# Kernel tuning notes

Measured on AMD Instinct MI355X. Metric: run time of the kernel, lower is better.

## Reference

```python
import jax, jax.numpy as jnp
from jax import lax
import numpy as np

VOCAB, HIDDEN, NUM_TAGS = 8000, 256, 4
B, T = 128, 512


def setup_inputs() -> dict:
    key = jax.random.key(0)
    ks = jax.random.split(key, 12)
    s_emb = 1.0
    s_conv = 1.0 / np.sqrt(HIDDEN * 3)
    s_dense = 1.0 / np.sqrt(HIDDEN)
    emb = jax.random.normal(ks[0], (VOCAB, HIDDEN), jnp.float32) * s_emb
    emb = emb.at[0].set(0.0)  # padding_idx=0
    inp = {
        'x': jax.random.randint(ks[1], (B, T), 0, VOCAB, jnp.int32),
        'y': jax.random.randint(ks[2], (B, T), 0, NUM_TAGS, jnp.int32),
        'mask': jnp.ones((B, T), jnp.bool_),
        'emb': emb,
        'w1': jax.random.normal(ks[3], (HIDDEN, HIDDEN, 3), jnp.float32) * s_conv,
        'b1': jnp.zeros((HIDDEN,), jnp.float32),
        'w2': jax.random.normal(ks[4], (HIDDEN, HIDDEN, 3), jnp.float32) * s_conv,
        'b2': jnp.zeros((HIDDEN,), jnp.float32),
        'w3': jax.random.normal(ks[5], (HIDDEN, HIDDEN, 3), jnp.float32) * s_conv,
        'b3': jnp.zeros((HIDDEN,), jnp.float32),
        'dense_w': jax.random.normal(ks[6], (NUM_TAGS, HIDDEN), jnp.float32) * s_dense,
        'dense_b': jnp.zeros((NUM_TAGS,), jnp.float32),
        'start_trans': jax.random.uniform(ks[7], (NUM_TAGS,), jnp.float32, -0.1, 0.1),
        'end_trans': jax.random.uniform(ks[8], (NUM_TAGS,), jnp.float32, -0.1, 0.1),
        'trans': jax.random.uniform(ks[9], (NUM_TAGS, NUM_TAGS), jnp.float32, -0.1, 0.1),
    }
    return inp


def _conv_relu(h, w, b):
    # h: [B, C, T]; replicate-pad 1 each side on time, kernel 3, stride 1
    hp = jnp.pad(h, ((0, 0), (0, 0), (1, 1)), mode='edge')
    out = lax.conv_general_dilated(hp, w, (1,), 'VALID',
                                   dimension_numbers=('NCH', 'OIH', 'NCH'))
    return jax.nn.relu(out + b[None, :, None])


def _crf_llh(em, tags, mask, start_trans, end_trans, trans):
    # em [B,T,L], tags [B,T], mask [B,T] float -> summed log-likelihood (torchcrf reduction='sum')
    bsz = em.shape[0]
    em_t = jnp.swapaxes(em, 0, 1)      # [T,B,L]
    tags_t = tags.T                    # [T,B]
    mask_t = mask.T                    # [T,B]
    bidx = jnp.arange(bsz)

    # numerator: score of the given tag sequence
    first = start_trans[tags_t[0]] + em_t[0, bidx, tags_t[0]]

    def num_step(carry, inp):
        score, prev = carry
        e, tg, m = inp
        s = trans[prev, tg] + e[bidx, tg]
        score = score + s * m
        prev = jnp.where(m > 0, tg, prev)
        return (score, prev), None

    (num, last_tag), _ = lax.scan(num_step, (first, tags_t[0]),
                                  (em_t[1:], tags_t[1:], mask_t[1:]))
    num = num + end_trans[last_tag]

    # denominator: forward algorithm (log partition)
    alpha0 = start_trans[None, :] + em_t[0]  # [B,L]

    def part_step(alpha, inp):
        e, m = inp
        nxt = jax.nn.logsumexp(alpha[:, :, None] + trans[None, :, :] + e[:, None, :], axis=1)
        return jnp.where(m[:, None] > 0, nxt, alpha), None

    alpha, _ = lax.scan(part_step, alpha0, (em_t[1:], mask_t[1:]))
    logz = jax.nn.logsumexp(alpha + end_trans[None, :], axis=1)
    return jnp.sum(num - logz)


def reference(x, y, mask, emb, w1, b1, w2, b2, w3, b3, dense_w, dense_b,
              start_trans, end_trans, trans):
    h = emb[x]                         # [B,T,H]
    h = jnp.swapaxes(h, 1, 2)          # [B,H,T]
    h = _conv_relu(h, w1, b1)
    h = _conv_relu(h, w2, b2)
    h = _conv_relu(h, w3, b3)
    h = jnp.swapaxes(h, 1, 2)          # [B,T,H]
    em = jnp.einsum('bth,lh->btl', h, dense_w) + dense_b
    m = mask.astype(em.dtype)
    return _crf_llh(em, y, m, start_trans, end_trans, trans)
```

## Files before the change

kernel.cpp:

```cpp
#include <hip/hip_runtime.h>
#include <hip/hip_bf16.h>
#include <hip/hip_fp8.h>

#define Bc 128
#define Tt 512
#define Hc 256
#define Lc 4
#define BM 128
#define APB 272
#define HR 134

typedef __attribute__((ext_vector_type(8))) short short8;
typedef __attribute__((ext_vector_type(4))) float f32x4;
typedef unsigned char uchar;
typedef unsigned long long u64;

__device__ __forceinline__ uchar f2f8(float f) {
    __hip_fp8_e4m3 q(f);
    return (uchar)q.__x;
}
__device__ __forceinline__ float f82f(uchar b) {
    __hip_fp8_e4m3 q; q.__x = (__hip_fp8_storage_t)b;
    return (float)q;
}

__global__ __launch_bounds__(256) void prep_emb(const float* __restrict__ e,
                                                uchar* __restrict__ eb)
{
    int i = blockIdx.x * 256 + threadIdx.x;
    const float4* s = (const float4*)(e + (size_t)i * 8);
    float4 a = s[0], b = s[1];
    u64 r = (u64)f2f8(a.x)
          | ((u64)f2f8(a.y) << 8)
          | ((u64)f2f8(a.z) << 16)
          | ((u64)f2f8(a.w) << 24)
          | ((u64)f2f8(b.x) << 32)
          | ((u64)f2f8(b.y) << 40)
          | ((u64)f2f8(b.z) << 48)
          | ((u64)f2f8(b.w) << 56);
    *(u64*)(eb + (size_t)i * 8) = r;
}

__global__ __launch_bounds__(256) void prep_w(const float* __restrict__ w,
                                              uchar* __restrict__ wbF)
{
    int i = blockIdx.x * 256 + threadIdx.x;
    int co = i / 768;
    int r  = i - co * 768;
    int ci = r / 3;
    int k  = r - ci * 3;
    int cib = ci >> 5, lk = (ci >> 3) & 3, e = ci & 7;
    wbF[(size_t)(k * 8 + cib) * 8192 + co * 32 + lk * 8 + e] = f2f8(w[i]);
}

__global__ __launch_bounds__(512) void fused_net(
    const uchar* __restrict__ embF, const int* __restrict__ x,
    const uchar* __restrict__ wbF,
    const float* __restrict__ b1, const float* __restrict__ b2,
    const float* __restrict__ b3,
    const float* __restrict__ dw, const float* __restrict__ db,
    float* __restrict__ em)
{
    __shared__ __align__(16) uchar Hb[HR * APB];

    const int b    = blockIdx.y;
    const int t0   = blockIdx.x * BM;
    const int tid  = threadIdx.x;
    const int lane = tid & 63, wid = tid >> 6;
    const int wm = wid >> 2, wn = wid & 3;
    const int lr = lane & 15, lk = lane >> 4;
    const bool first = (blockIdx.x == 0), last = (blockIdx.x == gridDim.x - 1);

    for (int ch = tid; ch < HR * 16; ch += 512) {
        int r = ch >> 4, c = ch & 15;
        int t = t0 - 3 + r;
        t = t < 0 ? 0 : (t > Tt - 1 ? Tt - 1 : t);
        int row = x[b * Tt + t];
        *(short8*)&Hb[r * APB + c * 16] =
            *(const short8*)&embF[(size_t)row * Hc + c * 16];
    }
    __syncthreads();

    const int blo = wn * 2048 + lr * 32 + lk * 8;
    const f32x4 fzero = {0.f, 0.f, 0.f, 0.f};

    for (int layer = 0; layer < 3; ++layer) {
        const uchar* wL = wbF + (size_t)layer * 24 * 8192;
        const float* bz = layer == 0 ? b1 : (layer == 1 ? b2 : b3);

        int ob[5];
        #pragma unroll
        for (int f = 0; f < 4; ++f) ob[f] = (1 + layer) + (wm * 4 + f) * 16;
        ob[4] = 117 - layer;

        f32x4 acc[5][4];
        #pragma unroll
        for (int f = 0; f < 5; ++f)
            #pragma unroll
            for (int ni = 0; ni < 4; ++ni) acc[f][ni] = fzero;

        long bp[3][4];
        #pragma unroll
        for (int ni = 0; ni < 4; ++ni)
            bp[0][ni] = *(const long*)&wL[blo + ni * 512];
        #pragma unroll
        for (int ni = 0; ni < 4; ++ni)
            bp[1][ni] = *(const long*)&wL[8192 + blo + ni * 512];

        long af[2][5];
        #pragma unroll
        for (int f = 0; f < 5; ++f)
            af[0][f] = *(const long*)&Hb[(ob[f] + lr - 1) * APB + lk * 8];

        #pragma unroll
        for (int s = 0; s < 24; ++s) {
            const int cur = s & 1;
            if (s + 2 < 24) {
                const uchar* nb = wL + (size_t)(s + 2) * 8192 + blo;
                #pragma unroll
                for (int ni = 0; ni < 4; ++ni)
                    bp[(s + 2) % 3][ni] = *(const long*)&nb[ni * 512];
            }
            if (s + 1 < 24) {
                const int k1 = (s + 1) >> 3, ci1 = ((s + 1) & 7) << 5;
                #pragma unroll
                for (int f = 0; f < 5; ++f)
                    af[cur ^ 1][f] = *(const long*)
                        &Hb[(ob[f] + lr + k1 - 1) * APB + ci1 + lk * 8];
            }
            #pragma unroll
            for (int f = 0; f < 5; ++f)
                #pragma unroll
                for (int ni = 0; ni < 4; ++ni)
                    acc[f][ni] = __builtin_amdgcn_mfma_f32_16x16x32_fp8_fp8(
                        af[cur][f], bp[s % 3][ni], acc[f][ni], 0, 0, 0);
        }
        __syncthreads();

        float bv[4];
        #pragma unroll
        for (int ni = 0; ni < 4; ++ni) bv[ni] = bz[wn * 64 + ni * 16 + lr];
        #pragma unroll
        for (int f = 0; f < 5; ++f)
            #pragma unroll
            for (int ni = 0; ni < 4; ++ni)
                #pragma unroll
                for (int j = 0; j < 4; ++j) {
                    int o  = ob[f] + lk * 4 + j;
                    int co = wn * 64 + ni * 16 + lr;
                    float v = acc[f][ni][j] + bv[ni];
                    v = v > 0.f ? v : 0.f;
                    Hb[o * APB + co] = f2f8(v);
                }
        __syncthreads();

        if (layer < 2) {
            if (first && tid < Hc) {
                uchar v = Hb[3 * APB + tid];
                Hb[2 * APB + tid] = v;
                if (layer == 0) Hb[1 * APB + tid] = v;
            }
            if (last && tid >= Hc) {
                int c = tid - Hc;
                uchar v = Hb[130 * APB + c];
                Hb[131 * APB + c] = v;
                if (layer == 0) Hb[132 * APB + c] = v;
            }
            __syncthreads();
        }
    }

    {
        int m = tid >> 2, l = tid & 3;
        float s = db[l];
        const uchar* hrow = &Hb[(3 + m) * APB];
        #pragma unroll 8
        for (int c8 = 0; c8 < 32; ++c8) {
            u64 hv = *(const u64*)&hrow[c8 * 8];
            const float4 w0 = *(const float4*)&dw[l * Hc + c8 * 8];
            const float4 w1 = *(const float4*)&dw[l * Hc + c8 * 8 + 4];
            s += f82f((uchar)(hv       )) * w0.x
               + f82f((uchar)(hv >>  8 )) * w0.y
               + f82f((uchar)(hv >> 16 )) * w0.z
               + f82f((uchar)(hv >> 24 )) * w0.w
               + f82f((uchar)(hv >> 32 )) * w1.x
               + f82f((uchar)(hv >> 40 )) * w1.y
               + f82f((uchar)(hv >> 48 )) * w1.z
               + f82f((uchar)(hv >> 56 )) * w1.w;
        }
        em[(size_t)(b * Tt + t0 + m) * Lc + l] = s;
    }
}

__device__ __forceinline__ float lse4(float x0, float x1, float x2, float x3) {
    float m = fmaxf(fmaxf(x0, x1), fmaxf(x2, x3));
    return m + __logf(__expf(x0 - m) + __expf(x1 - m) +
                      __expf(x2 - m) + __expf(x3 - m));
}
__device__ __forceinline__ float self4(int k, float4 v) {
    return k == 0 ? v.x : (k == 1 ? v.y : (k == 2 ? v.z : v.w));
}

__global__ __launch_bounds__(64) void crf_scan(
    const float* __restrict__ em, const int* __restrict__ y,
    const float* __restrict__ start_t, const float* __restrict__ end_t,
    const float* __restrict__ trans, float* __restrict__ llh)
{
    const int b    = blockIdx.x;
    const int lane = threadIdx.x;

    float Tm[4][4];
    #pragma unroll
    for (int i = 0; i < 4; ++i) {
        float4 r = *(const float4*)&trans[i * 4];
        Tm[i][0] = r.x; Tm[i][1] = r.y; Tm[i][2] = r.z; Tm[i][3] = r.w;
    }

    const float4* emrow = (const float4*)(em + (size_t)b * Tt * Lc);
    const int*    yb    = y + (size_t)b * Tt;

    const int ts = 8 * lane + 1;
    const int te = min(ts + 8, Tt);

    float P[4][4];
    {
        float4 ev = emrow[ts];
        float e[4] = {ev.x, ev.y, ev.z, ev.w};
        #pragma unroll
        for (int i = 0; i < 4; ++i)
            #pragma unroll
            for (int j = 0; j < 4; ++j)
                P[i][j] = Tm[i][j] + e[j];
    }
    float num = trans[yb[ts - 1] * 4 + yb[ts]] + self4(yb[ts], emrow[ts]);

    for (int t = ts + 1; t < te; ++t) {
        float4 ev = emrow[t];
        float e[4] = {ev.x, ev.y, ev.z, ev.w};
        num += trans[yb[t - 1] * 4 + yb[t]] + self4(yb[t], ev);
        float C[4][4];
        #pragma unroll
        for (int i = 0; i < 4; ++i)
            #pragma unroll
            for (int j = 0; j < 4; ++j)
                C[i][j] = lse4(P[i][0] + Tm[0][j], P[i][1] + Tm[1][j],
                               P[i][2] + Tm[2][j], P[i][3] + Tm[3][j]) + e[j];
        #pragma unroll
        for (int i = 0; i < 4; ++i)
            #pragma unroll
            for (int j = 0; j < 4; ++j) P[i][j] = C[i][j];
    }

    {
        float4 e0 = emrow[0];
        if (lane == 0)  num += self4(yb[0], e0) + start_t[yb[0]];
        if (lane == 63) num += end_t[yb[Tt - 1]];
    }

    #pragma unroll
    for (int d = 0; d < 6; ++d) {
        const int bit = 1 << d;
        const bool left = (lane & bit) == 0;
        float Bm[4][4];
        #pragma unroll
        for (int i = 0; i < 4; ++i)
            #pragma unroll
            for (int j = 0; j < 4; ++j)
                Bm[i][j] = __shfl_xor(P[i][j], bit, 64);
        float C[4][4];
        #pragma unroll
        for (int i = 0; i < 4; ++i)
            #pragma unroll
            for (int j = 0; j < 4; ++j) {
                float x0 = (left ? P[i][0] : Bm[i][0]) + (left ? Bm[0][j] : P[0][j]);
                float x1 = (left ? P[i][1] : Bm[i][1]) + (left ? Bm[1][j] : P[1][j]);
                float x2 = (left ? P[i][2] : Bm[i][2]) + (left ? Bm[2][j] : P[2][j]);
                float x3 = (left ? P[i][3] : Bm[i][3]) + (left ? Bm[3][j] : P[3][j]);
                C[i][j] = lse4(x0, x1, x2, x3);
            }
        #pragma unroll
        for (int i = 0; i < 4; ++i)
            #pragma unroll
            for (int j = 0; j < 4; ++j) P[i][j] = C[i][j];
    }

    #pragma unroll
    for (int off = 32; off; off >>= 1) num += __shfl_xor(num, off, 64);

    if (lane == 0) {
        float4 e0 = emrow[0];
        float a0 = start_t[0] + e0.x, a1 = start_t[1] + e0.y;
        float a2 = start_t[2] + e0.z, a3 = start_t[3] + e0.w;
        float aF[4];
        #pragma unroll
        for (int j = 0; j < 4; ++j)
            aF[j] = lse4(a0 + P[0][j], a1 + P[1][j], a2 + P[2][j], a3 + P[3][j]);
        float logz = lse4(aF[0] + end_t[0], aF[1] + end_t[1],
                          aF[2] + end_t[2], aF[3] + end_t[3]);
        llh[b] = num - logz;
    }
}

__global__ __launch_bounds__(64) void final_reduce(const float* __restrict__ llh,
                                                   float* __restrict__ out)
{
    int l = threadIdx.x;
    float v = llh[l] + llh[l + 64];
    #pragma unroll
    for (int off = 32; off; off >>= 1) v += __shfl_down(v, off);
    if (l == 0) out[0] = v;
}

extern "C" void kernel_launch(void* const* d_in, const int* in_sizes, int n_in,
                              void* d_out, int out_size, void* d_ws, size_t ws_size,
                              hipStream_t stream) {
    const int*   x    = (const int*)d_in[0];
    const int*   y    = (const int*)d_in[1];
    const float* emb  = (const float*)d_in[3];
    const float* w1   = (const float*)d_in[4];
    const float* b1   = (const float*)d_in[5];
    const float* w2   = (const float*)d_in[6];
    const float* b2   = (const float*)d_in[7];
    const float* w3   = (const float*)d_in[8];
    const float* b3   = (const float*)d_in[9];
    const float* dw   = (const float*)d_in[10];
    const float* db   = (const float*)d_in[11];
    const float* st   = (const float*)d_in[12];
    const float* en   = (const float*)d_in[13];
    const float* tr   = (const float*)d_in[14];
    float* out = (float*)d_out;

    uchar* wbF  = (uchar*)d_ws;
    uchar* embF = wbF + 3 * 24 * 8192;
    float* em   = (float*)(embF + 8000 * Hc);
    float* llh  = em + (size_t)Bc * Tt * Lc;

    prep_w<<<768, 256, 0, stream>>>(w1, wbF);
    prep_w<<<768, 256, 0, stream>>>(w2, wbF + 24 * 8192);
    prep_w<<<768, 256, 0, stream>>>(w3, wbF + 48 * 8192);
    prep_emb<<<1000, 256, 0, stream>>>(emb, embF);

    dim3 grid(Tt / BM, Bc);
    fused_net<<<grid, 512, 0, stream>>>(embF, x, wbF, b1, b2, b3, dw, db, em);

    crf_scan<<<Bc, 64, 0, stream>>>(em, y, st, en, tr, llh);
    final_reduce<<<1, 64, 0, stream>>>(llh, out);
}
```

Measured before the change: 141.0 us.

## Shrink fused conv tile to 32 timesteps with 4-wave blocks for occupancy

Cuts the per-block time tile from 128 to 32 rows and the block from 512 to 256 threads. Each wave now owns a 64-channel output slice across all rows, computing 3 (or 2 in the last layer) 16-row fragments, and the double-buffered A-fragment prefetch is dropped. The grid grows fourfold, which spreads work across more CUs and raises occupancy. In exchange, halo recompute per output row increases, and every block re-streams the full fp8 weight set from cache, multiplying weight traffic and lowering MFMA reuse per B load.

```diff
diff --git a/kernel.cpp b/kernel.cpp
--- a/kernel.cpp
+++ b/kernel.cpp
@@ -6,9 +6,9 @@
 #define Tt 512
 #define Hc 256
 #define Lc 4
-#define BM 128
+#define BM 32
 #define APB 272
-#define HR 134
+#define HR 38
 
 typedef __attribute__((ext_vector_type(8))) short short8;
 typedef __attribute__((ext_vector_type(4))) float f32x4;
@@ -53,7 +53,7 @@
     wbF[(size_t)(k * 8 + cib) * 8192 + co * 32 + lk * 8 + e] = f2f8(w[i]);
 }
 
-__global__ __launch_bounds__(512) void fused_net(
+__global__ __launch_bounds__(256) void fused_net(
     const uchar* __restrict__ embF, const int* __restrict__ x,
     const uchar* __restrict__ wbF,
     const float* __restrict__ b1, const float* __restrict__ b2,
@@ -66,12 +66,12 @@
     const int b    = blockIdx.y;
     const int t0   = blockIdx.x * BM;
     const int tid  = threadIdx.x;
-    const int lane = tid & 63, wid = tid >> 6;
-    const int wm = wid >> 2, wn = wid & 3;
+    const int lane = tid & 63;
+    const int wn   = tid >> 6;
     const int lr = lane & 15, lk = lane >> 4;
     const bool first = (blockIdx.x == 0), last = (blockIdx.x == gridDim.x - 1);
 
-    for (int ch = tid; ch < HR * 16; ch += 512) {
+    for (int ch = tid; ch < HR * 16; ch += 256) {
         int r = ch >> 4, c = ch & 15;
         int t = t0 - 3 + r;
         t = t < 0 ? 0 : (t > Tt - 1 ? Tt - 1 : t);
@@ -87,15 +87,14 @@
     for (int layer = 0; layer < 3; ++layer) {
         const uchar* wL = wbF + (size_t)layer * 24 * 8192;
         const float* bz = layer == 0 ? b1 : (layer == 1 ? b2 : b3);
-
-        int ob[5];
-        #pragma unroll
-        for (int f = 0; f < 4; ++f) ob[f] = (1 + layer) + (wm * 4 + f) * 16;
-        ob[4] = 117 - layer;
-
-        f32x4 acc[5][4];
-        #pragma unroll
-        for (int f = 0; f < 5; ++f)
+        const int nf = (layer == 2) ? 2 : 3;
+
+        int ob[3];
+        ob[0] = 1 + layer; ob[1] = 17 + layer; ob[2] = 21 - layer;
+
+        f32x4 acc[3][4];
+        #pragma unroll
+        for (int f = 0; f < 3; ++f)
             #pragma unroll
             for (int ni = 0; ni < 4; ++ni) acc[f][ni] = fzero;
 
@@ -107,70 +106,65 @@
         for (int ni = 0; ni < 4; ++ni)
             bp[1][ni] = *(const long*)&wL[8192 + blo + ni * 512];
 
-        long af[2][5];
-        #pragma unroll
-        for (int f = 0; f < 5; ++f)
-            af[0][f] = *(const long*)&Hb[(ob[f] + lr - 1) * APB + lk * 8];
-
         #pragma unroll
         for (int s = 0; s < 24; ++s) {
-            const int cur = s & 1;
             if (s + 2 < 24) {
                 const uchar* nb = wL + (size_t)(s + 2) * 8192 + blo;
                 #pragma unroll
                 for (int ni = 0; ni < 4; ++ni)
                     bp[(s + 2) % 3][ni] = *(const long*)&nb[ni * 512];
             }
-            if (s + 1 < 24) {
-                const int k1 = (s + 1) >> 3, ci1 = ((s + 1) & 7) << 5;
-                #pragma unroll
-                for (int f = 0; f < 5; ++f)
-                    af[cur ^ 1][f] = *(const long*)
-                        &Hb[(ob[f] + lr + k1 - 1) * APB + ci1 + lk * 8];
-            }
-            #pragma unroll
-            for (int f = 0; f < 5; ++f)
+            const int k = s >> 3, ci0 = (s & 7) << 5;
+            long af[3];
+            #pragma unroll
+            for (int f = 0; f < 3; ++f)
+                if (f < nf)
+                    af[f] = *(const long*)
+                        &Hb[(ob[f] + lr + k - 1) * APB + ci0 + lk * 8];
+            #pragma unroll
+            for (int f = 0; f < 3; ++f)
+                if (f < nf)
+                    #pragma unroll
+                    for (int ni = 0; ni < 4; ++ni)
+                        acc[f][ni] = __builtin_amdgcn_mfma_f32_16x16x32_fp8_fp8(
+                            af[f], bp[s % 3][ni], acc[f][ni], 0, 0, 0);
+        }
+        __syncthreads();
+
+        float bv[4];
+        #pragma unroll
+        for (int ni = 0; ni < 4; ++ni) bv[ni] = bz[wn * 64 + ni * 16 + lr];
+        #pragma unroll
+        for (int f = 0; f < 3; ++f)
+            if (f < nf)
                 #pragma unroll
                 for (int ni = 0; ni < 4; ++ni)
-                    acc[f][ni] = __builtin_amdgcn_mfma_f32_16x16x32_fp8_fp8(
-                        af[cur][f], bp[s % 3][ni], acc[f][ni], 0, 0, 0);
-        }
+                    #pragma unroll
+                    for (int j = 0; j < 4; ++j) {
+                        int o  = ob[f] + lk * 4 + j;
+                        int co = wn * 64 + ni * 16 + lr;
+                        float v = acc[f][ni][j] + bv[ni];
+                        v = v > 0.f ? v : 0.f;
+                        Hb[o * APB + co] = f2f8(v);
+                    }
         __syncthreads();
 
-        float bv[4];
-        #pragma unroll
-        for (int ni = 0; ni < 4; ++ni) bv[ni] = bz[wn * 64 + ni * 16 + lr];
-        #pragma unroll
-        for (int f = 0; f < 5; ++f)
-            #pragma unroll
-            for (int ni = 0; ni < 4; ++ni)
-                #pragma unroll
-                for (int j = 0; j < 4; ++j) {
-                    int o  = ob[f] + lk * 4 + j;
-                    int co = wn * 64 + ni * 16 + lr;
-                    float v = acc[f][ni][j] + bv[ni];
-                    v = v > 0.f ? v : 0.f;
-                    Hb[o * APB + co] = f2f8(v);
-                }
-        __syncthreads();
-
         if (layer < 2) {
-            if (first && tid < Hc) {
+            if (first) {
                 uchar v = Hb[3 * APB + tid];
                 Hb[2 * APB + tid] = v;
                 if (layer == 0) Hb[1 * APB + tid] = v;
             }
-            if (last && tid >= Hc) {
-                int c = tid - Hc;
-                uchar v = Hb[130 * APB + c];
-                Hb[131 * APB + c] = v;
-                if (layer == 0) Hb[132 * APB + c] = v;
+            if (last) {
+                uchar v = Hb[34 * APB + tid];
+                Hb[35 * APB + tid] = v;
+                if (layer == 0) Hb[36 * APB + tid] = v;
             }
-            __syncthreads();
+            if (first || last) __syncthreads();
         }
     }
 
-    {
+    if (tid < 4 * BM) {
         int m = tid >> 2, l = tid & 3;
         float s = db[l];
         const uchar* hrow = &Hb[(3 + m) * APB];
@@ -341,7 +335,7 @@
     prep_emb<<<1000, 256, 0, stream>>>(emb, embF);
 
     dim3 grid(Tt / BM, Bc);
-    fused_net<<<grid, 512, 0, stream>>>(embF, x, wbF, b1, b2, b3, dw, db, em);
+    fused_net<<<grid, 256, 0, stream>>>(embF, x, wbF, b1, b2, b3, dw, db, em);
 
     crf_scan<<<Bc, 64, 0, stream>>>(em, y, st, en, tr, llh);
     final_reduce<<<1, 64, 0, stream>>>(llh, out);
```

New measurement: 148.3 us. 1.05x slower.
